# Kernel optimization log

Measured on AMD Instinct MI355X. Metric: run time of the kernel, lower is better.

Reference implementation:

```python
import jax, jax.numpy as jnp
import numpy as np

DIM = 128   # EMBED_DIM
NH = 4      # N_HEADS
HD = DIM // NH          # 32
NT = max(1, int(NH * 0.25))  # 1 timelike head
NS = NH - NT                 # 3 spacelike heads
TD = NT * HD                 # T_DIM = 32
SD = 6      # STATE_DIM
TIN, TOUT = 20, 20
NL = 3      # N_LAYERS
B, T = 4096, TIN + TOUT      # seq len capped by pos embedding (40)


def _ln(x, g, b):
    m = jnp.mean(x, -1, keepdims=True)
    v = jnp.mean((x - m) ** 2, -1, keepdims=True)
    return g * (x - m) * jax.lax.rsqrt(v + 1e-5) + b


def _mln(x, pg, pb, g, b):
    # MinkowskiLN: standard LN then scale by |sum(s^2)-sum(t^2)| norm
    x = _ln(x, pg, pb)
    t = x[..., :TD]
    s = x[..., TD:]
    mq = jnp.sum(s * s, -1, keepdims=True) - jnp.sum(t * t, -1, keepdims=True)
    eps = jnp.maximum(0.01 * jnp.mean(jnp.abs(mq)), 1e-5)
    return g * (x / (jnp.sqrt(jnp.abs(mq) + eps) + eps)) + b


def _attn(h, qt, kt, qs, ks, vw, ow, ob, ws):
    # Minkowski attention (mode='f3'): timelike scores negated with learned sigmoid weight
    Bb, Tt, _ = h.shape
    scale = HD ** -0.5
    Qt = (h @ qt).reshape(Bb, Tt, NT, HD)
    Kt = (h @ kt).reshape(Bb, Tt, NT, HD)
    Qs = (h @ qs).reshape(Bb, Tt, NS, HD)
    Ks = (h @ ks).reshape(Bb, Tt, NS, HD)
    st = jnp.einsum('bthd,bshd->bths', Qt, Kt)  # [B,T,NT,T]
    ss = jnp.einsum('bthd,bshd->bths', Qs, Ks)  # [B,T,NS,T]
    score = jnp.concatenate([-jax.nn.sigmoid(ws) * st, ss], axis=2) * scale
    a = jax.nn.softmax(score, axis=-1)
    V = (h @ vw).reshape(Bb, Tt, NH, HD)
    o = jnp.einsum('bths,bshd->bthd', a, V).reshape(Bb, Tt, DIM)
    return o @ ow + ob


def setup_inputs() -> dict:
    key = jax.random.key(0)
    ks = iter(jax.random.split(key, 32))
    def w(shape, s=0.02):
        return (jax.random.normal(next(ks), shape, jnp.float32) * s).astype(jnp.float32)
    inp = {
        'x': jax.random.normal(next(ks), (B, T, SD), jnp.float32),
        'embed_w': w((SD, DIM)), 'embed_b': jnp.zeros((DIM,), jnp.float32),
        'pos': w((TIN + TOUT, DIM)),
        'qt_w': w((NL, DIM, NT * HD)), 'kt_w': w((NL, DIM, NT * HD)),
        'qs_w': w((NL, DIM, NS * HD)), 'ks_w': w((NL, DIM, NS * HD)),
        'v_w': w((NL, DIM, DIM)), 'out_w': w((NL, DIM, DIM)), 'out_b': jnp.zeros((NL, DIM), jnp.float32),
        'w_sigma': jnp.zeros((NL,), jnp.float32),
        'n1_pre_g': jnp.ones((NL, DIM), jnp.float32), 'n1_pre_b': jnp.zeros((NL, DIM), jnp.float32),
        'n1_g': jnp.ones((NL, DIM), jnp.float32), 'n1_b': jnp.zeros((NL, DIM), jnp.float32),
        'n2_pre_g': jnp.ones((NL, DIM), jnp.float32), 'n2_pre_b': jnp.zeros((NL, DIM), jnp.float32),
        'n2_g': jnp.ones((NL, DIM), jnp.float32), 'n2_b': jnp.zeros((NL, DIM), jnp.float32),
        'ff_w1': w((NL, DIM, 4 * DIM)), 'ff_b1': jnp.zeros((NL, 4 * DIM), jnp.float32),
        'ff_w2': w((NL, 4 * DIM, DIM)), 'ff_b2': jnp.zeros((NL, DIM), jnp.float32),
        'fn_pre_g': jnp.ones((DIM,), jnp.float32), 'fn_pre_b': jnp.zeros((DIM,), jnp.float32),
        'fn_g': jnp.ones((DIM,), jnp.float32), 'fn_b': jnp.zeros((DIM,), jnp.float32),
        'traj_w': w((DIM, SD * TOUT)), 'traj_b': jnp.zeros((SD * TOUT,), jnp.float32),
    }
    return inp


def reference(x, embed_w, embed_b, pos, qt_w, kt_w, qs_w, ks_w, v_w, out_w, out_b,
              w_sigma, n1_pre_g, n1_pre_b, n1_g, n1_b, n2_pre_g, n2_pre_b, n2_g, n2_b,
              ff_w1, ff_b1, ff_w2, ff_b2, fn_pre_g, fn_pre_b, fn_g, fn_b, traj_w, traj_b):
    Tt = x.shape[1]
    h = x @ embed_w + embed_b + pos[:Tt]  # [B,T,D]
    for i in range(NL):
        h = h + _attn(_mln(h, n1_pre_g[i], n1_pre_b[i], n1_g[i], n1_b[i]),
                      qt_w[i], kt_w[i], qs_w[i], ks_w[i], v_w[i], out_w[i], out_b[i], w_sigma[i])
        hn = _mln(h, n2_pre_g[i], n2_pre_b[i], n2_g[i], n2_b[i])
        h = h + (jax.nn.gelu(hn @ ff_w1[i] + ff_b1[i], approximate=False) @ ff_w2[i] + ff_b2[i])
    h = _mln(h, fn_pre_g, fn_pre_b, fn_g, fn_b)[:, -1, :]  # [B,D]
    out = h @ traj_w + traj_b
    return out.reshape(x.shape[0], TOUT, SD)
```

## Files before the change

kernel.cpp:

```cpp
#include <hip/hip_runtime.h>
#include <hip/hip_bf16.h>

#define DIMM 128
#define TT   40
#define BB   4096
#define NTOK (BB*TT)
#define NLAY 3

typedef float f4 __attribute__((ext_vector_type(4)));
typedef float f32x4 __attribute__((ext_vector_type(4)));
typedef short bf16x8 __attribute__((ext_vector_type(8)));

__device__ __forceinline__ float bf2f(unsigned short u) {
    union { unsigned int i; float f; } v; v.i = ((unsigned int)u) << 16; return v.f;
}
__device__ __forceinline__ unsigned short f2bu(float f) {
    __hip_bfloat16 h = __float2bfloat16(f);
    return *reinterpret_cast<unsigned short*>(&h);
}
__device__ __forceinline__ float gelu_f(float v) {
    float z = 1.5957691216057308f * fmaf(0.044715f * v * v, v, v);
    return v / (1.f + __expf(-z));
}

__device__ __forceinline__ void mln_rowstat(
    const float* v, const float* pgv, const float* pbv,
    float& m, float& rstd, float& mq)
{
    float s1 = 0.f, s2 = 0.f;
    #pragma unroll
    for (int nf = 0; nf < 8; ++nf) { s1 += v[nf]; s2 += v[nf]*v[nf]; }
    #pragma unroll
    for (int o = 1; o < 16; o <<= 1) { s1 += __shfl_xor(s1, o); s2 += __shfl_xor(s2, o); }
    m = s1 * (1.f/128.f);
    float var = s2 * (1.f/128.f) - m*m;
    rstd = rsqrtf(fmaxf(var, 0.f) + 1e-5f);
    float q = 0.f;
    #pragma unroll
    for (int nf = 0; nf < 8; ++nf) {
        float yv = (v[nf] - m) * rstd * pgv[nf] + pbv[nf];
        q += (nf < 2 ? -(yv*yv) : (yv*yv));
    }
    #pragma unroll
    for (int o = 1; o < 16; o <<= 1) q += __shfl_xor(q, o);
    mq = q;
}

__device__ __forceinline__ void build_mln_frags(
    bf16x8 a[2][4], const float* __restrict__ h, int row_mf0, int row_mf1,
    const float* __restrict__ stats, float eps,
    const float* __restrict__ pg, const float* __restrict__ pb,
    const float* __restrict__ gg, const float* __restrict__ gb, int q)
{
    int rows[2] = { row_mf0, row_mf1 };
    float rss3[2], mm[2], s3v[2];
    #pragma unroll
    for (int mf = 0; mf < 2; ++mf) {
        int r = rows[mf];
        float m  = stats[(size_t)r*4 + 0];
        float rs = stats[(size_t)r*4 + 1];
        float mq = stats[(size_t)r*4 + 2];
        float s3 = 1.f / (sqrtf(fabsf(mq) + eps) + eps);
        rss3[mf] = rs * s3; mm[mf] = -m * rss3[mf]; s3v[mf] = s3;
    }
    #pragma unroll
    for (int ks = 0; ks < 4; ++ks) {
        int c0 = ks*32 + q*8;
        float al[8], be[8], gbv[8];
        #pragma unroll
        for (int j = 0; j < 8; ++j) {
            float g = gg[c0+j];
            al[j] = g * pg[c0+j]; be[j] = g * pb[c0+j]; gbv[j] = gb[c0+j];
        }
        #pragma unroll
        for (int mf = 0; mf < 2; ++mf) {
            int r = rows[mf];
            f4 x0 = *(const f4*)(h + (size_t)r*128 + c0);
            f4 x1 = *(const f4*)(h + (size_t)r*128 + c0 + 4);
            union { unsigned short u[8]; bf16x8 v; } o;
            #pragma unroll
            for (int j = 0; j < 4; ++j) {
                float t0 = fmaf(x0[j], rss3[mf], mm[mf]);
                float t1 = fmaf(x1[j], rss3[mf], mm[mf]);
                o.u[j]   = f2bu(fmaf(al[j],   t0, fmaf(be[j],   s3v[mf], gbv[j])));
                o.u[j+4] = f2bu(fmaf(al[j+4], t1, fmaf(be[j+4], s3v[mf], gbv[j+4])));
            }
            a[mf][ks] = o.v;
        }
    }
}

__global__ __launch_bounds__(256) void pack_w_k(
    const float* __restrict__ qt, const float* __restrict__ kt,
    const float* __restrict__ qs, const float* __restrict__ ks,
    const float* __restrict__ vw, const float* __restrict__ ow,
    const float* __restrict__ w1, const float* __restrict__ w2,
    unsigned short* __restrict__ wqT, unsigned short* __restrict__ outT,
    unsigned short* __restrict__ ff1T, unsigned short* __restrict__ ff2T)
{
    int idx = blockIdx.x * 256 + threadIdx.x;
    if (idx < 147456) {
        int i = idx / 49152, r = idx % 49152;
        int n = r / 128, k = r % 128;
        float v;
        if (n < 32)        v = qt[i*4096  + k*32  + n];
        else if (n < 64)   v = kt[i*4096  + k*32  + (n-32)];
        else if (n < 160)  v = qs[i*12288 + k*96  + (n-64)];
        else if (n < 256)  v = ks[i*12288 + k*96  + (n-160)];
        else               v = vw[i*16384 + k*128 + (n-256)];
        wqT[idx] = f2bu(v);
    } else if (idx < 196608) {
        int j = idx - 147456;
        int i = j / 16384, r = j % 16384;
        int n = r / 128, k = r % 128;
        outT[j] = f2bu(ow[i*16384 + k*128 + n]);
    } else if (idx < 393216) {
        int j = idx - 196608;
        int i = j / 65536, r = j % 65536;
        int n = r / 128, k = r % 128;
        ff1T[j] = f2bu(w1[i*65536 + k*512 + n]);
    } else {
        int j = idx - 393216;
        int i = j / 65536, r = j % 65536;
        int n = r / 512, k = r % 512;
        ff2T[j] = f2bu(w2[i*65536 + k*128 + n]);
    }
}

__global__ __launch_bounds__(256) void embed_k(
    const float* __restrict__ x, const float* __restrict__ ew,
    const float* __restrict__ eb, const float* __restrict__ pos,
    float* __restrict__ h)
{
    int idx = blockIdx.x * 256 + threadIdx.x;
    int n = idx >> 7, d = idx & 127;
    int t = n % TT;
    const float* xr = x + (size_t)n * 6;
    float acc = eb[d] + pos[t*128 + d];
    #pragma unroll
    for (int k = 0; k < 6; ++k) acc += xr[k] * ew[k*128 + d];
    h[idx] = acc;
}

__global__ __launch_bounds__(256) void mln_stats_k(
    const float* __restrict__ h, const float* __restrict__ pg, const float* __restrict__ pb,
    float* __restrict__ stats, float* __restrict__ partials)
{
    int wid = threadIdx.x >> 6, lane = threadIdx.x & 63;
    int tok = blockIdx.x * 4 + wid;
    const float* hr = h + (size_t)tok * 128;
    float x0 = hr[lane], x1 = hr[lane + 64];
    float s = x0 + x1;
    #pragma unroll
    for (int o = 32; o > 0; o >>= 1) s += __shfl_xor(s, o);
    float m = s * (1.f / 128.f);
    float d0 = x0 - m, d1 = x1 - m;
    float v = d0*d0 + d1*d1;
    #pragma unroll
    for (int o = 32; o > 0; o >>= 1) v += __shfl_xor(v, o);
    float rstd = rsqrtf(v * (1.f / 128.f) + 1e-5f);
    float y0 = d0 * rstd * pg[lane]      + pb[lane];
    float y1 = d1 * rstd * pg[lane + 64] + pb[lane + 64];
    float q = (lane < 32 ? -(y0*y0) : (y0*y0)) + y1*y1;
    #pragma unroll
    for (int o = 32; o > 0; o >>= 1) q += __shfl_xor(q, o);
    if (lane == 0) {
        stats[(size_t)tok*4 + 0] = m;
        stats[(size_t)tok*4 + 1] = rstd;
        stats[(size_t)tok*4 + 2] = q;
    }
    __shared__ float pm[4];
    if (lane == 0) pm[wid] = fabsf(q);
    __syncthreads();
    if (threadIdx.x == 0) partials[blockIdx.x] = (pm[0] + pm[1]) + (pm[2] + pm[3]);
}

__global__ __launch_bounds__(1024) void reduce_eps_k(
    const float* __restrict__ partials, int n, float* __restrict__ scal)
{
    float s = 0.f;
    for (int i = threadIdx.x; i < n; i += 1024) s += partials[i];
    __shared__ float sm[1024];
    sm[threadIdx.x] = s;
    __syncthreads();
    for (int o = 512; o > 0; o >>= 1) {
        if (threadIdx.x < o) sm[threadIdx.x] += sm[threadIdx.x + o];
        __syncthreads();
    }
    if (threadIdx.x == 0) {
        float mean = sm[0] / (float)NTOK;
        scal[0] = fmaxf(0.01f * mean, 1e-5f);
    }
}

__global__ __launch_bounds__(256) void qkv_k(
    const float* __restrict__ hsrc,
    const float* __restrict__ stats_in, const float* __restrict__ scal,
    const float* __restrict__ pg, const float* __restrict__ pb,
    const float* __restrict__ gg, const float* __restrict__ gb,
    const unsigned short* __restrict__ BT,
    unsigned short* __restrict__ obuf)
{
    __shared__ unsigned char Wl[32768];
    const int tid = threadIdx.x, wid = tid >> 6, lane = tid & 63;
    const int q = lane >> 4, l15 = lane & 15;
    const int row0 = blockIdx.x * 128;
    const int wrow = row0 + wid * 32;

    bf16x8 a[2][4];
    build_mln_frags(a, hsrc, wrow + l15, wrow + 16 + l15,
                    stats_in, scal[0], pg, pb, gg, gb, q);

    const unsigned char* BTb = (const unsigned char*)BT;
    for (int nc = 0; nc < 3; ++nc) {
        __syncthreads();
        {
            int row = tid >> 1, half = tid & 1;
            #pragma unroll
            for (int jj = 0; jj < 8; ++jj) {
                int colb = half*128 + jj*16;
                uint4 v = *(const uint4*)(BTb + (size_t)(nc*128 + row)*256 + colb);
                *(uint4*)(Wl + row*256 + (colb ^ ((row & 7) << 4))) = v;
            }
        }
        __syncthreads();
        f32x4 acc[2][8] = {};
        #pragma unroll
        for (int ks = 0; ks < 4; ++ks)
            #pragma unroll
            for (int nf = 0; nf < 8; ++nf) {
                int row = nf*16 + l15;
                bf16x8 b = *(const bf16x8*)(Wl + row*256 + ((ks*64 + q*16) ^ ((row & 7) << 4)));
                #pragma unroll
                for (int mf = 0; mf < 2; ++mf)
                    acc[mf][nf] = __builtin_amdgcn_mfma_f32_16x16x32_bf16(a[mf][ks], b, acc[mf][nf], 0, 0, 0);
            }
        #pragma unroll
        for (int mf = 0; mf < 2; ++mf)
            #pragma unroll
            for (int r = 0; r < 4; ++r) {
                int row = wrow + mf*16 + q*4 + r;
                #pragma unroll
                for (int nf = 0; nf < 8; ++nf)
                    obuf[(size_t)row*384 + nc*128 + nf*16 + l15] = f2bu(acc[mf][nf][r]);
            }
    }
}

__global__ __launch_bounds__(256) void attn_k(
    unsigned short* __restrict__ scratch, const float* __restrict__ wsp)
{
    __shared__ unsigned char VtL[16384];
    __shared__ unsigned char PlL[24576];
    const int b = blockIdx.x, tid = threadIdx.x;
    unsigned short* base = scratch + (size_t)b * TT * 384;

    for (int e = tid; e < 1536; e += 256) {
        int hh = e / 384, rem = e - hh*384;
        int row = rem >> 3, c = rem & 7;
        int byte = hh*6144 + ((row*128 + 96 + 4*c) ^ ((row & 7) << 4));
        *(unsigned int*)(PlL + byte) = 0u;
    }
    for (int e = tid; e < 1536; e += 256) {
        int hh = e / 384, rem = e - hh*384;
        int d = rem / 12, sc2 = rem - d*12;
        int s = 40 + 2*sc2;
        int byte = hh*4096 + ((d*128 + s*2) ^ (((d >> 3) & 7) << 4));
        *(unsigned int*)(VtL + byte) = 0u;
    }
    for (int e = tid; e < 640; e += 256) {
        int s = e >> 4, ck = e & 15;
        union { bf16x8 v; unsigned short u[8]; } g;
        g.v = *(const bf16x8*)(base + (size_t)s*384 + 256 + ck*8);
        int hh = ck >> 2, d0 = (ck & 3) * 8;
        #pragma unroll
        for (int j = 0; j < 8; ++j) {
            int d = d0 + j;
            int byte = hh*4096 + ((d*128 + s*2) ^ (((d >> 3) & 7) << 4));
            *(unsigned short*)(VtL + byte) = g.u[j];
        }
    }
    __syncthreads();

    const int h = tid >> 6, lane = tid & 63;
    const int l15 = lane & 15, q4 = lane >> 4;
    const unsigned char* Vt = VtL + h*4096;
    unsigned char* Pl = PlL + h*6144;

    const int qcol = (h == 0) ? 0  : 32  + h*32;
    const int kcol = (h == 0) ? 32 : 128 + h*32;
    const float scale = 0.17677669529663687f;
    const float wmul = (h == 0) ? (-scale / (1.f + __expf(-wsp[0]))) : scale;

    bf16x8 aq[3], bk[3];
    #pragma unroll
    for (int mt = 0; mt < 3; ++mt) {
        int t = l15 + 16*mt; if (t > 39) t = 39;
        aq[mt] = *(const bf16x8*)(base + (size_t)t*384 + qcol + q4*8);
    }
    #pragma unroll
    for (int jt = 0; jt < 3; ++jt) {
        int s = l15 + 16*jt; if (s > 39) s = 39;
        bk[jt] = *(const bf16x8*)(base + (size_t)s*384 + kcol + q4*8);
    }
    f32x4 sc[3][3] = {};
    #pragma unroll
    for (int mt = 0; mt < 3; ++mt)
        #pragma unroll
        for (int jt = 0; jt < 3; ++jt)
            sc[mt][jt] = __builtin_amdgcn_mfma_f32_16x16x32_bf16(aq[mt], bk[jt], sc[mt][jt], 0, 0, 0);

    const bool mask2 = (l15 >= 8);
    float inv[3][4];
    #pragma unroll
    for (int mt = 0; mt < 3; ++mt) {
        #pragma unroll
        for (int r = 0; r < 4; ++r) {
            float s0 = wmul * sc[mt][0][r];
            float s1 = wmul * sc[mt][1][r];
            float s2 = mask2 ? -1e30f : wmul * sc[mt][2][r];
            float mx = fmaxf(fmaxf(s0, s1), s2);
            #pragma unroll
            for (int o = 1; o < 16; o <<= 1) mx = fmaxf(mx, __shfl_xor(mx, o));
            float e0 = __expf(s0 - mx), e1 = __expf(s1 - mx), e2 = __expf(s2 - mx);
            float sum = e0 + e1 + e2;
            #pragma unroll
            for (int o = 1; o < 16; o <<= 1) sum += __shfl_xor(sum, o);
            inv[mt][r] = 1.f / sum;
            int row = 16*mt + 4*q4 + r;
            int rsw = (row & 7) << 4;
            *(unsigned short*)(Pl + ((row*128 + l15*2       ) ^ rsw)) = f2bu(e0);
            *(unsigned short*)(Pl + ((row*128 + 32 + l15*2  ) ^ rsw)) = f2bu(e1);
            *(unsigned short*)(Pl + ((row*128 + 64 + l15*2  ) ^ rsw)) = f2bu(e2);
        }
    }

    f32x4 oacc[3][2] = {};
    #pragma unroll
    for (int ks2 = 0; ks2 < 2; ++ks2) {
        bf16x8 bv[2];
        #pragma unroll
        for (int nt = 0; nt < 2; ++nt) {
            int d = l15 + 16*nt;
            bv[nt] = *(const bf16x8*)(Vt + ((d*128 + 64*ks2 + 16*q4) ^ (((d >> 3) & 7) << 4)));
        }
        #pragma unroll
        for (int mt = 0; mt < 3; ++mt) {
            int row = l15 + 16*mt;
            bf16x8 pa = *(const bf16x8*)(Pl + ((row*128 + 64*ks2 + 16*q4) ^ ((row & 7) << 4)));
            #pragma unroll
            for (int nt = 0; nt < 2; ++nt)
                oacc[mt][nt] = __builtin_amdgcn_mfma_f32_16x16x32_bf16(pa, bv[nt], oacc[mt][nt], 0, 0, 0);
        }
    }
    #pragma unroll
    for (int mt = 0; mt < 3; ++mt) {
        #pragma unroll
        for (int r = 0; r < 4; ++r) {
            int t = 16*mt + 4*q4 + r;
            if (t < 40) {
                float iv = inv[mt][r];
                unsigned short* orow = base + (size_t)t*384 + 256 + h*32;
                orow[l15]      = f2bu(oacc[mt][0][r] * iv);
                orow[l15 + 16] = f2bu(oacc[mt][1][r] * iv);
            }
        }
    }
}

__global__ __launch_bounds__(64) void outproj_k(
    const unsigned short* __restrict__ scratch,
    const unsigned short* __restrict__ BT,
    const float* __restrict__ bias,
    float* __restrict__ hres,
    const float* __restrict__ pre_g, const float* __restrict__ pre_b,
    float* __restrict__ stats, float* __restrict__ partials)
{
    const int lane = threadIdx.x;
    const int q = lane >> 4, l15 = lane & 15;
    const int row0 = blockIdx.x * 32;

    bf16x8 a[2][4];
    #pragma unroll
    for (int mf = 0; mf < 2; ++mf) {
        int row = row0 + mf*16 + l15;
        #pragma unroll
        for (int ks = 0; ks < 4; ++ks)
            a[mf][ks] = *(const bf16x8*)(scratch + (size_t)row*384 + 256 + ks*32 + q*8);
    }

    f32x4 acc[2][8] = {};
    #pragma unroll
    for (int ks = 0; ks < 4; ++ks)
        #pragma unroll
        for (int nf = 0; nf < 8; ++nf) {
            bf16x8 b = *(const bf16x8*)(BT + (size_t)(nf*16 + l15)*128 + ks*32 + q*8);
            #pragma unroll
            for (int mf = 0; mf < 2; ++mf)
                acc[mf][nf] = __builtin_amdgcn_mfma_f32_16x16x32_bf16(a[mf][ks], b, acc[mf][nf], 0, 0, 0);
        }

    float bv[8], pgv[8], pbv[8];
    #pragma unroll
    for (int nf = 0; nf < 8; ++nf) {
        int c = nf*16 + l15;
        bv[nf] = bias[c]; pgv[nf] = pre_g[c]; pbv[nf] = pre_b[c];
    }
    float amq = 0.f;
    #pragma unroll
    for (int mf = 0; mf < 2; ++mf) {
        #pragma unroll
        for (int r = 0; r < 4; ++r) {
            int row = row0 + mf*16 + q*4 + r;
            float* hr = hres + (size_t)row*128;
            float v[8];
            #pragma unroll
            for (int nf = 0; nf < 8; ++nf) {
                float hv = hr[nf*16 + l15] + acc[mf][nf][r] + bv[nf];
                hr[nf*16 + l15] = hv;
                v[nf] = hv;
            }
            float m, rstd, mq;
            mln_rowstat(v, pgv, pbv, m, rstd, mq);
            if (l15 == 0) {
                stats[(size_t)row*4 + 0] = m;
                stats[(size_t)row*4 + 1] = rstd;
                stats[(size_t)row*4 + 2] = mq;
            }
            amq += fabsf(mq);
        }
    }
    amq += __shfl_xor(amq, 16);
    amq += __shfl_xor(amq, 32);
    if (lane == 0) partials[blockIdx.x] = amq;
}

__global__ __launch_bounds__(256) void ffn_k(
    const float* __restrict__ hsrc,
    const float* __restrict__ stats_in, const float* __restrict__ scal,
    const float* __restrict__ m2_pre_g, const float* __restrict__ m2_pre_b,
    const float* __restrict__ m2_g, const float* __restrict__ m2_b,
    const unsigned short* __restrict__ W1T,
    const float* __restrict__ b1,
    const unsigned short* __restrict__ W2T,
    const float* __restrict__ b2,
    float* __restrict__ h,
    const float* __restrict__ pre_g, const float* __restrict__ pre_b,
    float* __restrict__ stats, float* __restrict__ partials)
{
    __shared__ unsigned char W1l[16384];
    __shared__ unsigned char W2l[16384];
    __shared__ unsigned char Ps[4][32*144];
    __shared__ float sm[16];
    const int tid = threadIdx.x, wid = tid >> 6, lane = tid & 63;
    const int q = lane >> 4, l15 = lane & 15;
    const int row0 = blockIdx.x * 128;
    const int wrow = row0 + wid * 32;
    unsigned char* Pw = Ps[wid];

    bf16x8 a[2][4];
    build_mln_frags(a, hsrc, wrow + l15, wrow + 16 + l15,
                    stats_in, scal[0], m2_pre_g, m2_pre_b, m2_g, m2_b, q);

    float b2v[8];
    #pragma unroll
    for (int nf = 0; nf < 8; ++nf) b2v[nf] = b2[nf*16 + l15];

    f32x4 acc2[2][8] = {};
    const unsigned char* W1b = (const unsigned char*)W1T;
    const unsigned char* W2b = (const unsigned char*)W2T;

    for (int c = 0; c < 8; ++c) {
        __syncthreads();
        {
            int row = tid >> 2, seg = tid & 3;
            #pragma unroll
            for (int jj = 0; jj < 4; ++jj) {
                int colb = seg*64 + jj*16;
                uint4 v = *(const uint4*)(W1b + (size_t)(c*64 + row)*256 + colb);
                *(uint4*)(W1l + row*256 + (colb ^ ((row & 7) << 4))) = v;
            }
        }
        {
            int row = tid >> 1, seg = tid & 1;
            #pragma unroll
            for (int jj = 0; jj < 4; ++jj) {
                int colb = seg*64 + jj*16;
                uint4 v = *(const uint4*)(W2b + (size_t)row*1024 + c*128 + colb);
                *(uint4*)(W2l + row*128 + (colb ^ ((row & 7) << 4))) = v;
            }
        }
        __syncthreads();
        f32x4 acc1[2][4] = {};
        #pragma unroll
        for (int ks = 0; ks < 4; ++ks)
            #pragma unroll
            for (int nf = 0; nf < 4; ++nf) {
                int row = nf*16 + l15;
                bf16x8 b = *(const bf16x8*)(W1l + row*256 + ((ks*64 + q*16) ^ ((row & 7) << 4)));
                #pragma unroll
                for (int mf = 0; mf < 2; ++mf)
                    acc1[mf][nf] = __builtin_amdgcn_mfma_f32_16x16x32_bf16(a[mf][ks], b, acc1[mf][nf], 0, 0, 0);
            }
        #pragma unroll
        for (int nf = 0; nf < 4; ++nf) {
            float bb = b1[c*64 + nf*16 + l15];
            #pragma unroll
            for (int mf = 0; mf < 2; ++mf) {
                #pragma unroll
                for (int r = 0; r < 4; ++r) {
                    float v = gelu_f(acc1[mf][nf][r] + bb);
                    *(unsigned short*)(Pw + (mf*16 + q*4 + r)*144 + (nf*16 + l15)*2) = f2bu(v);
                }
            }
        }
        #pragma unroll
        for (int ks2 = 0; ks2 < 2; ++ks2) {
            bf16x8 a2[2];
            #pragma unroll
            for (int mf = 0; mf < 2; ++mf)
                a2[mf] = *(const bf16x8*)(Pw + (mf*16 + l15)*144 + ks2*64 + q*16);
            #pragma unroll
            for (int nf = 0; nf < 8; ++nf) {
                int row = nf*16 + l15;
                bf16x8 b = *(const bf16x8*)(W2l + row*128 + ((ks2*64 + q*16) ^ ((row & 7) << 4)));
                #pragma unroll
                for (int mf = 0; mf < 2; ++mf)
                    acc2[mf][nf] = __builtin_amdgcn_mfma_f32_16x16x32_bf16(a2[mf], b, acc2[mf][nf], 0, 0, 0);
            }
        }
    }

    float pgv[8], pbv[8];
    #pragma unroll
    for (int nf = 0; nf < 8; ++nf) { pgv[nf] = pre_g[nf*16 + l15]; pbv[nf] = pre_b[nf*16 + l15]; }
    float amq = 0.f;
    #pragma unroll
    for (int mf = 0; mf < 2; ++mf) {
        #pragma unroll
        for (int r = 0; r < 4; ++r) {
            int row = wrow + mf*16 + q*4 + r;
            float* hr = h + (size_t)row*128;
            float v[8];
            #pragma unroll
            for (int nf = 0; nf < 8; ++nf) {
                float hv = hr[nf*16 + l15] + acc2[mf][nf][r] + b2v[nf];
                hr[nf*16 + l15] = hv;
                v[nf] = hv;
            }
            float m, rstd, mq;
            mln_rowstat(v, pgv, pbv, m, rstd, mq);
            if (l15 == 0) {
                stats[(size_t)row*4 + 0] = m;
                stats[(size_t)row*4 + 1] = rstd;
                stats[(size_t)row*4 + 2] = mq;
            }
            amq += fabsf(mq);
        }
    }
    if (l15 == 0) sm[wid*4 + q] = amq;
    __syncthreads();
    if (tid == 0) {
        float s = 0.f;
        #pragma unroll
        for (int j = 0; j < 16; ++j) s += sm[j];
        partials[blockIdx.x] = s;
    }
}

__global__ __launch_bounds__(128) void head_k(
    const float* __restrict__ h, const float* __restrict__ stats, const float* __restrict__ scal,
    const float* __restrict__ pg, const float* __restrict__ pb,
    const float* __restrict__ gg, const float* __restrict__ gb,
    const float* __restrict__ tw, const float* __restrict__ tb,
    float* __restrict__ out)
{
    int b = blockIdx.x, tid = threadIdx.x;
    int tok = b*TT + (TT - 1);
    __shared__ float ys[128];
    float eps = scal[0];
    float m  = stats[(size_t)tok*4 + 0];
    float rs = stats[(size_t)tok*4 + 1];
    float mq = stats[(size_t)tok*4 + 2];
    float s3 = 1.f / (sqrtf(fabsf(mq) + eps) + eps);
    float x = h[(size_t)tok*128 + tid];
    ys[tid] = gg[tid] * (((x - m) * rs * pg[tid] + pb[tid]) * s3) + gb[tid];
    __syncthreads();
    if (tid < 120) {
        float acc = tb[tid];
        #pragma unroll 4
        for (int d = 0; d < 128; ++d) acc += ys[d] * tw[d*120 + tid];
        out[(size_t)b*120 + tid] = acc;
    }
}

extern "C" void kernel_launch(void* const* d_in, const int* in_sizes, int n_in,
                              void* d_out, int out_size, void* d_ws, size_t ws_size,
                              hipStream_t stream) {
    const float* x        = (const float*)d_in[0];
    const float* embed_w  = (const float*)d_in[1];
    const float* embed_b  = (const float*)d_in[2];
    const float* pos      = (const float*)d_in[3];
    const float* qt_w     = (const float*)d_in[4];
    const float* kt_w     = (const float*)d_in[5];
    const float* qs_w     = (const float*)d_in[6];
    const float* ks_w     = (const float*)d_in[7];
    const float* v_w      = (const float*)d_in[8];
    const float* out_w    = (const float*)d_in[9];
    const float* out_b    = (const float*)d_in[10];
    const float* w_sigma  = (const float*)d_in[11];
    const float* n1_pre_g = (const float*)d_in[12];
    const float* n1_pre_b = (const float*)d_in[13];
    const float* n1_g     = (const float*)d_in[14];
    const float* n1_b     = (const float*)d_in[15];
    const float* n2_pre_g = (const float*)d_in[16];
    const float* n2_pre_b = (const float*)d_in[17];
    const float* n2_g     = (const float*)d_in[18];
    const float* n2_b     = (const float*)d_in[19];
    const float* ff_w1    = (const float*)d_in[20];
    const float* ff_b1    = (const float*)d_in[21];
    const float* ff_w2    = (const float*)d_in[22];
    const float* ff_b2    = (const float*)d_in[23];
    const float* fn_pre_g = (const float*)d_in[24];
    const float* fn_pre_b = (const float*)d_in[25];
    const float* fn_g     = (const float*)d_in[26];
    const float* fn_b     = (const float*)d_in[27];
    const float* traj_w   = (const float*)d_in[28];
    const float* traj_b   = (const float*)d_in[29];

    char* ws = (char*)d_ws;
    float*          h        = (float*)ws;
    float*          stats    = (float*)(ws + 83886080);
    unsigned short* scratch  = (unsigned short*)(ws + 86507520);
    unsigned short* wqT      = (unsigned short*)(ws + 212336640);
    unsigned short* outT     = (unsigned short*)(ws + 212631552);
    unsigned short* ff1T     = (unsigned short*)(ws + 212729856);
    unsigned short* ff2T     = (unsigned short*)(ws + 213123072);
    float*          partials = (float*)(ws + 213516288);
    float*          scal     = (float*)(ws + 213680128);

    pack_w_k<<<2304, 256, 0, stream>>>(qt_w, kt_w, qs_w, ks_w, v_w, out_w, ff_w1, ff_w2,
                                       wqT, outT, ff1T, ff2T);
    embed_k<<<81920, 256, 0, stream>>>(x, embed_w, embed_b, pos, h);

    mln_stats_k<<<40960, 256, 0, stream>>>(h, n1_pre_g, n1_pre_b, stats, partials);
    reduce_eps_k<<<1, 1024, 0, stream>>>(partials, 40960, scal);

    for (int i = 0; i < NLAY; ++i) {
        qkv_k<<<1280, 256, 0, stream>>>(
            h, stats, scal,
            n1_pre_g + i*128, n1_pre_b + i*128, n1_g + i*128, n1_b + i*128,
            wqT + (size_t)i*49152, scratch);
        attn_k<<<4096, 256, 0, stream>>>(scratch, w_sigma + i);
        outproj_k<<<5120, 64, 0, stream>>>(
            scratch, outT + (size_t)i*16384, out_b + i*128,
            h, n2_pre_g + i*128, n2_pre_b + i*128,
            stats, partials);
        reduce_eps_k<<<1, 1024, 0, stream>>>(partials, 5120, scal);
        const float* npg = (i < NLAY-1) ? (n1_pre_g + (i+1)*128) : fn_pre_g;
        const float* npb = (i < NLAY-1) ? (n1_pre_b + (i+1)*128) : fn_pre_b;
        ffn_k<<<1280, 256, 0, stream>>>(
            h, stats, scal,
            n2_pre_g + i*128, n2_pre_b + i*128, n2_g + i*128, n2_b + i*128,
            ff1T + (size_t)i*65536, ff_b1 + i*512,
            ff2T + (size_t)i*65536, ff_b2 + i*128, h,
            npg, npb, stats, partials);
        reduce_eps_k<<<1, 1024, 0, stream>>>(partials, 1280, scal);
    }

    head_k<<<4096, 128, 0, stream>>>(h, stats, scal, fn_pre_g, fn_pre_b, fn_g, fn_b,
                                     traj_w, traj_b, (float*)d_out);
}
```

Baseline: 972.5 us.

## Fuse output projection and residual/MinkowskiLN stats into attention kernel

The attention kernel now keeps its per-sequence output in LDS, loads the out-projection weights into shared memory, and performs the out-projection GEMM, bias, residual add and next-LN row statistics itself, writing per-block partials. This removes the separate outproj kernel launch and the round trip of the attention output through global scratch. Separately, the FFN first-layer bias is folded into the accumulator initialisation. Costs include a larger LDS footprint per block, an extra barrier, and only 3 of 4 waves doing the projection work.

Result: faster. 909.0 us, median of 2 (-6.5%).

```diff
diff --git a/kernel.cpp b/kernel.cpp
--- a/kernel.cpp
+++ b/kernel.cpp
@@ -248,12 +248,20 @@
 }
 
 __global__ __launch_bounds__(256) void attn_k(
-    unsigned short* __restrict__ scratch, const float* __restrict__ wsp)
-{
-    __shared__ unsigned char VtL[16384];
-    __shared__ unsigned char PlL[24576];
+    const unsigned short* __restrict__ scratch, const float* __restrict__ wsp,
+    const unsigned short* __restrict__ outT,
+    const float* __restrict__ bias,
+    float* __restrict__ hres,
+    const float* __restrict__ pre_g, const float* __restrict__ pre_b,
+    float* __restrict__ stats, float* __restrict__ partials)
+{
+    __shared__ unsigned char lds[45056];
+    __shared__ float sm[16];
     const int b = blockIdx.x, tid = threadIdx.x;
-    unsigned short* base = scratch + (size_t)b * TT * 384;
+    const unsigned short* base = scratch + (size_t)b * TT * 384;
+
+    unsigned char* VtL = lds;
+    unsigned char* PlL = lds + 16384;
 
     for (int e = tid; e < 1536; e += 256) {
         int hh = e / 384, rem = e - hh*384;
@@ -353,86 +361,93 @@
                 oacc[mt][nt] = __builtin_amdgcn_mfma_f32_16x16x32_bf16(pa, bv[nt], oacc[mt][nt], 0, 0, 0);
         }
     }
+
+    __syncthreads();
+    unsigned char* Ol = lds;
+    unsigned char* Wl = lds + 12288;
+
     #pragma unroll
     for (int mt = 0; mt < 3; ++mt) {
         #pragma unroll
         for (int r = 0; r < 4; ++r) {
-            int t = 16*mt + 4*q4 + r;
+            int row = 16*mt + 4*q4 + r;
+            float iv = inv[mt][r];
+            int rsw = (row & 7) << 4;
+            #pragma unroll
+            for (int nt = 0; nt < 2; ++nt) {
+                int colb = (h*32 + nt*16 + l15) * 2;
+                *(unsigned short*)(Ol + ((row*256 + colb) ^ rsw)) = f2bu(oacc[mt][nt][r] * iv);
+            }
+        }
+    }
+    {
+        const unsigned char* BTb = (const unsigned char*)outT;
+        int row = tid >> 1, half = tid & 1;
+        #pragma unroll
+        for (int jj = 0; jj < 8; ++jj) {
+            int colb = half*128 + jj*16;
+            uint4 v = *(const uint4*)(BTb + (size_t)row*256 + colb);
+            *(uint4*)(Wl + row*256 + (colb ^ ((row & 7) << 4))) = v;
+        }
+    }
+    if (h == 3 && l15 == 0) sm[12 + q4] = 0.f;
+    __syncthreads();
+
+    if (h < 3) {
+        int arow = 16*h + l15;
+        bf16x8 ao[4];
+        #pragma unroll
+        for (int ks = 0; ks < 4; ++ks)
+            ao[ks] = *(const bf16x8*)(Ol + arow*256 + ((ks*64 + q4*16) ^ ((arow & 7) << 4)));
+        f32x4 oc[8] = {};
+        #pragma unroll
+        for (int ks = 0; ks < 4; ++ks)
+            #pragma unroll
+            for (int nf = 0; nf < 8; ++nf) {
+                int brow = nf*16 + l15;
+                bf16x8 bo = *(const bf16x8*)(Wl + brow*256 + ((ks*64 + q4*16) ^ ((brow & 7) << 4)));
+                oc[nf] = __builtin_amdgcn_mfma_f32_16x16x32_bf16(ao[ks], bo, oc[nf], 0, 0, 0);
+            }
+
+        float bv[8], pgv[8], pbv[8];
+        #pragma unroll
+        for (int nf = 0; nf < 8; ++nf) {
+            int c = nf*16 + l15;
+            bv[nf] = bias[c]; pgv[nf] = pre_g[c]; pbv[nf] = pre_b[c];
+        }
+        float amq = 0.f;
+        #pragma unroll
+        for (int r = 0; r < 4; ++r) {
+            int t = 16*h + 4*q4 + r;
             if (t < 40) {
-                float iv = inv[mt][r];
-                unsigned short* orow = base + (size_t)t*384 + 256 + h*32;
-                orow[l15]      = f2bu(oacc[mt][0][r] * iv);
-                orow[l15 + 16] = f2bu(oacc[mt][1][r] * iv);
-            }
-        }
-    }
-}
-
-__global__ __launch_bounds__(64) void outproj_k(
-    const unsigned short* __restrict__ scratch,
-    const unsigned short* __restrict__ BT,
-    const float* __restrict__ bias,
-    float* __restrict__ hres,
-    const float* __restrict__ pre_g, const float* __restrict__ pre_b,
-    float* __restrict__ stats, float* __restrict__ partials)
-{
-    const int lane = threadIdx.x;
-    const int q = lane >> 4, l15 = lane & 15;
-    const int row0 = blockIdx.x * 32;
-
-    bf16x8 a[2][4];
-    #pragma unroll
-    for (int mf = 0; mf < 2; ++mf) {
-        int row = row0 + mf*16 + l15;
-        #pragma unroll
-        for (int ks = 0; ks < 4; ++ks)
-            a[mf][ks] = *(const bf16x8*)(scratch + (size_t)row*384 + 256 + ks*32 + q*8);
-    }
-
-    f32x4 acc[2][8] = {};
-    #pragma unroll
-    for (int ks = 0; ks < 4; ++ks)
-        #pragma unroll
-        for (int nf = 0; nf < 8; ++nf) {
-            bf16x8 b = *(const bf16x8*)(BT + (size_t)(nf*16 + l15)*128 + ks*32 + q*8);
-            #pragma unroll
-            for (int mf = 0; mf < 2; ++mf)
-                acc[mf][nf] = __builtin_amdgcn_mfma_f32_16x16x32_bf16(a[mf][ks], b, acc[mf][nf], 0, 0, 0);
-        }
-
-    float bv[8], pgv[8], pbv[8];
-    #pragma unroll
-    for (int nf = 0; nf < 8; ++nf) {
-        int c = nf*16 + l15;
-        bv[nf] = bias[c]; pgv[nf] = pre_g[c]; pbv[nf] = pre_b[c];
-    }
-    float amq = 0.f;
-    #pragma unroll
-    for (int mf = 0; mf < 2; ++mf) {
-        #pragma unroll
-        for (int r = 0; r < 4; ++r) {
-            int row = row0 + mf*16 + q*4 + r;
-            float* hr = hres + (size_t)row*128;
-            float v[8];
-            #pragma unroll
-            for (int nf = 0; nf < 8; ++nf) {
-                float hv = hr[nf*16 + l15] + acc[mf][nf][r] + bv[nf];
-                hr[nf*16 + l15] = hv;
-                v[nf] = hv;
-            }
-            float m, rstd, mq;
-            mln_rowstat(v, pgv, pbv, m, rstd, mq);
-            if (l15 == 0) {
-                stats[(size_t)row*4 + 0] = m;
-                stats[(size_t)row*4 + 1] = rstd;
-                stats[(size_t)row*4 + 2] = mq;
-            }
-            amq += fabsf(mq);
-        }
-    }
-    amq += __shfl_xor(amq, 16);
-    amq += __shfl_xor(amq, 32);
-    if (lane == 0) partials[blockIdx.x] = amq;
+                int row = b*TT + t;
+                float* hr = hres + (size_t)row*128;
+                float v[8];
+                #pragma unroll
+                for (int nf = 0; nf < 8; ++nf) {
+                    float hv = hr[nf*16 + l15] + oc[nf][r] + bv[nf];
+                    hr[nf*16 + l15] = hv;
+                    v[nf] = hv;
+                }
+                float m, rstd, mq;
+                mln_rowstat(v, pgv, pbv, m, rstd, mq);
+                if (l15 == 0) {
+                    stats[(size_t)row*4 + 0] = m;
+                    stats[(size_t)row*4 + 1] = rstd;
+                    stats[(size_t)row*4 + 2] = mq;
+                }
+                amq += fabsf(mq);
+            }
+        }
+        if (l15 == 0) sm[h*4 + q4] = amq;
+    }
+    __syncthreads();
+    if (tid == 0) {
+        float s = 0.f;
+        #pragma unroll
+        for (int j = 0; j < 16; ++j) s += sm[j];
+        partials[b] = s;
+    }
 }
 
 __global__ __launch_bounds__(256) void ffn_k(
@@ -491,7 +506,15 @@
             }
         }
         __syncthreads();
-        f32x4 acc1[2][4] = {};
+        float bbv[4];
+        #pragma unroll
+        for (int nf = 0; nf < 4; ++nf) bbv[nf] = b1[c*64 + nf*16 + l15];
+        f32x4 acc1[2][4];
+        #pragma unroll
+        for (int mf = 0; mf < 2; ++mf)
+            #pragma unroll
+            for (int nf = 0; nf < 4; ++nf)
+                acc1[mf][nf] = f32x4{bbv[nf], bbv[nf], bbv[nf], bbv[nf]};
         #pragma unroll
         for (int ks = 0; ks < 4; ++ks)
             #pragma unroll
@@ -504,12 +527,11 @@
             }
         #pragma unroll
         for (int nf = 0; nf < 4; ++nf) {
-            float bb = b1[c*64 + nf*16 + l15];
             #pragma unroll
             for (int mf = 0; mf < 2; ++mf) {
                 #pragma unroll
                 for (int r = 0; r < 4; ++r) {
-                    float v = gelu_f(acc1[mf][nf][r] + bb);
+                    float v = gelu_f(acc1[mf][nf][r]);
                     *(unsigned short*)(Pw + (mf*16 + q*4 + r)*144 + (nf*16 + l15)*2) = f2bu(v);
                 }
             }
@@ -651,12 +673,12 @@
             h, stats, scal,
             n1_pre_g + i*128, n1_pre_b + i*128, n1_g + i*128, n1_b + i*128,
             wqT + (size_t)i*49152, scratch);
-        attn_k<<<4096, 256, 0, stream>>>(scratch, w_sigma + i);
-        outproj_k<<<5120, 64, 0, stream>>>(
-            scratch, outT + (size_t)i*16384, out_b + i*128,
+        attn_k<<<4096, 256, 0, stream>>>(
+            scratch, w_sigma + i,
+            outT + (size_t)i*16384, out_b + i*128,
             h, n2_pre_g + i*128, n2_pre_b + i*128,
             stats, partials);
-        reduce_eps_k<<<1, 1024, 0, stream>>>(partials, 5120, scal);
+        reduce_eps_k<<<1, 1024, 0, stream>>>(partials, 4096, scal);
         const float* npg = (i < NLAY-1) ? (n1_pre_g + (i+1)*128) : fn_pre_g;
         const float* npb = (i < NLAY-1) ? (n1_pre_b + (i+1)*128) : fn_pre_b;
         ffn_k<<<1280, 256, 0, stream>>>(
```
